# Kernel tuning notes

Measured on AMD Instinct MI355X. Metric: run time of the kernel, lower is better.

## Reference

```python
import jax, jax.numpy as jnp
import numpy as np

NEG_BIG = -9e15  # matches torch's -9000000000000000.0 masked-fill value
ALPHA = 0.2      # LeakyReLU negative slope


def setup_inputs() -> dict:
    key = jax.random.key(0)
    k1, k2, k3, k4 = jax.random.split(key, 4)
    N, F_in, F_out = 8192, 128, 64
    h = jax.random.normal(k1, (N, F_in), dtype=jnp.float32)
    adj = jax.random.randint(k2, (N, N), 0, 2).astype(jnp.float32)
    # Glorot(gain=1.414)-scale params
    W = jax.random.normal(k3, (F_in, F_out), dtype=jnp.float32) * (1.414 * np.sqrt(2.0 / (F_in + F_out)))
    a = jax.random.normal(k4, (2 * F_out, 1), dtype=jnp.float32) * (1.414 * np.sqrt(2.0 / (2 * F_out + 1)))
    return {"h": h, "adj": adj, "W": W, "a": a}


def reference(h, adj, W, a):
    F_out = W.shape[1]
    Wh = h @ W                               # [N, F_out]
    Wh1 = Wh @ a[:F_out, :]                  # [N, 1]
    Wh2 = Wh @ a[F_out:, :]                  # [N, 1]
    e = jax.nn.leaky_relu(Wh1 + Wh2.T, negative_slope=ALPHA)  # [N, N]
    attention = jnp.where(adj > 0, e, NEG_BIG)
    attention = jax.nn.softmax(attention, axis=1)
    # dropout omitted (eval mode / p applied only in training)
    h_prime = attention @ Wh                 # [N, F_out]
    return jax.nn.elu(h_prime)               # concat=True -> ELU
```

## Files before the change

### kernel.cpp

```cpp
#include <hip/hip_runtime.h>
#include <hip/hip_bf16.h>

#define N 8192
#define FIN 128
#define FOUT 64
#define ALPHA 0.2f
#define LOG2E 1.44269504f
#define JSPLIT 4
#define JSPAN (N / JSPLIT)
#define RBITS 65

typedef __attribute__((ext_vector_type(8))) short short8;
typedef __attribute__((ext_vector_type(4))) float f32x4;

static __device__ __forceinline__ unsigned fkey(float x) {
    unsigned u = __float_as_uint(x);
    return (u >> 31) ? ~u : (u | 0x80000000u);
}
static __device__ __forceinline__ float fdecode(unsigned k) {
    unsigned u = (k & 0x80000000u) ? (k & 0x7FFFFFFFu) : ~k;
    return __uint_as_float(u);
}

__global__ __launch_bounds__(256) void k_prep(const float* __restrict__ h,
                                              const float* __restrict__ W,
                                              const float* __restrict__ a,
                                              float* __restrict__ Wh,
                                              float* __restrict__ s2,
                                              float* __restrict__ t2,
                                              unsigned* __restrict__ keys) {
    __shared__ float lH[16 * FIN];
    __shared__ float lW[FIN * FOUT];
    __shared__ float red[8];
    const int tid = threadIdx.x;
    const int r0 = blockIdx.x * 16;
    {
        const float4* src = (const float4*)(h + (size_t)r0 * FIN);
        float4* dst = (float4*)lH;
        for (int i = tid; i < 16 * FIN / 4; i += 256) dst[i] = src[i];
        const float4* ws_ = (const float4*)W;
        float4* dw = (float4*)lW;
        for (int i = tid; i < FIN * FOUT / 4; i += 256) dw[i] = ws_[i];
    }
    __syncthreads();
    const int wave = tid >> 6, lane = tid & 63;
    float acc[4] = {0.f, 0.f, 0.f, 0.f};
    for (int k = 0; k < FIN; ++k) {
        float wv = lW[k * FOUT + lane];
#pragma unroll
        for (int r = 0; r < 4; ++r)
            acc[r] = fmaf(lH[(wave * 4 + r) * FIN + k], wv, acc[r]);
    }
    const float a1 = a[lane], a2 = a[FOUT + lane];
    float smx = -1e30f, tmx = -1e30f;
#pragma unroll
    for (int r = 0; r < 4; ++r) {
        int row = r0 + wave * 4 + r;
        Wh[(size_t)row * FOUT + lane] = acc[r];
        float sv = acc[r] * a1, tv = acc[r] * a2;
#pragma unroll
        for (int off = 32; off; off >>= 1) {
            sv += __shfl_xor(sv, off);
            tv += __shfl_xor(tv, off);
        }
        sv *= LOG2E; tv *= LOG2E;
        if (lane == 0) { s2[row] = sv; t2[row] = tv; }
        smx = fmaxf(smx, sv);
        tmx = fmaxf(tmx, tv);
    }
    if (lane == 0) { red[wave] = smx; red[4 + wave] = tmx; }
    __syncthreads();
    if (tid == 0) {
        float ms = fmaxf(fmaxf(red[0], red[1]), fmaxf(red[2], red[3]));
        float mt = fmaxf(fmaxf(red[4], red[5]), fmaxf(red[6], red[7]));
        atomicMax(keys + 0, fkey(ms));
        atomicMax(keys + 1, fkey(mt));
    }
}

__global__ __launch_bounds__(256) void k_pack(const float* __restrict__ Wh,
                                              __hip_bfloat16* __restrict__ WhB) {
    const int c = blockIdx.x;
    const int tn = threadIdx.x >> 6;
    const int lane = threadIdx.x & 63;
    const int quad = lane >> 4, l16 = lane & 15;
    const float* src = Wh + ((size_t)(c * 32 + quad * 8)) * FOUT + tn * 16 + l16;
    union { unsigned short u[8]; short8 v; } frag;
#pragma unroll
    for (int e = 0; e < 8; ++e) {
        __hip_bfloat16 b = __float2bfloat16(src[(size_t)e * FOUT]);
        frag.u[e] = *(unsigned short*)&b;
    }
    *(short8*)&WhB[(((size_t)c * 4 + tn) * 64 + lane) * 8] = frag.v;
}

__global__ __launch_bounds__(256) void k_bits(const float* __restrict__ adj,
                                              unsigned char* __restrict__ bits) {
    const size_t tb = (size_t)blockIdx.x * 256 + threadIdx.x;
    const float4* src = (const float4*)adj + tb * 2;
    float4 a = src[0];
    float4 b = src[1];
    unsigned m = 0;
    m |= (a.x != 0.f) ? 1u : 0u;
    m |= (a.y != 0.f) ? 2u : 0u;
    m |= (a.z != 0.f) ? 4u : 0u;
    m |= (a.w != 0.f) ? 8u : 0u;
    m |= (b.x != 0.f) ? 16u : 0u;
    m |= (b.y != 0.f) ? 32u : 0u;
    m |= (b.z != 0.f) ? 64u : 0u;
    m |= (b.w != 0.f) ? 128u : 0u;
    bits[tb] = (unsigned char)m;
}

__global__ __launch_bounds__(256) void k_attn(const unsigned* __restrict__ bits,
                                              const __hip_bfloat16* __restrict__ WhB,
                                              const float* __restrict__ s2,
                                              const float* __restrict__ t2,
                                              const unsigned* __restrict__ keys,
                                              float* __restrict__ acc_ws,
                                              float* __restrict__ l_ws) {
    __shared__ unsigned bitw[32 * RBITS];
    __shared__ float tl[JSPAN];
    __shared__ float ep[4][4][64][4];
    const int tid = threadIdx.x;
    const int wave = tid >> 6, lane = tid & 63;
    const int quad = lane >> 4, l16 = lane & 15;
    const int rg = wave >> 1, jh = wave & 1;
    const int i0 = blockIdx.x * 32;
    const int jb = blockIdx.y * JSPAN;

    for (int i = tid; i < 32 * 64; i += 256) {
        const int r = i >> 6, c = i & 63;
        bitw[r * RBITS + c] = bits[(size_t)(i0 + r) * (N / 32) + (jb >> 5) + c];
    }
    for (int i = tid; i < JSPAN / 4; i += 256)
        ((float4*)tl)[i] = ((const float4*)(t2 + jb))[i];
    __syncthreads();

    const float mraw = fdecode(keys[0]) + fdecode(keys[1]);
    const float mm = mraw > 0.f ? mraw : ALPHA * mraw;
    const int rrow = 16 * rg + l16;
    const float sm = s2[i0 + rrow];
    const short8* BF = (const short8*)WhB;
    const short8 onesv = {0x3F80, 0x3F80, 0x3F80, 0x3F80, 0x3F80, 0x3F80, 0x3F80, 0x3F80};

    f32x4 acc0 = {0,0,0,0}, acc1 = {0,0,0,0}, acc2 = {0,0,0,0}, acc3 = {0,0,0,0};
    f32x4 accL = {0,0,0,0};

    short8 Bp0[4], Bp1[4];

#define LOADB0(uu)                                                               \
    do {                                                                         \
        const int u_ = jh * 32 + ((uu) > 31 ? 31 : (uu));                        \
        const size_t kc_ = ((size_t)blockIdx.y * (JSPAN / 32) + u_) * 4;         \
        Bp0[0] = BF[(kc_ + 0) * 64 + lane];                                      \
        Bp0[1] = BF[(kc_ + 1) * 64 + lane];                                      \
        Bp0[2] = BF[(kc_ + 2) * 64 + lane];                                      \
        Bp0[3] = BF[(kc_ + 3) * 64 + lane];                                      \
    } while (0)
#define LOADB1(uu)                                                               \
    do {                                                                         \
        const int u_ = jh * 32 + ((uu) > 31 ? 31 : (uu));                        \
        const size_t kc_ = ((size_t)blockIdx.y * (JSPAN / 32) + u_) * 4;         \
        Bp1[0] = BF[(kc_ + 0) * 64 + lane];                                      \
        Bp1[1] = BF[(kc_ + 1) * 64 + lane];                                      \
        Bp1[2] = BF[(kc_ + 2) * 64 + lane];                                      \
        Bp1[3] = BF[(kc_ + 3) * 64 + lane];                                      \
    } while (0)
#define PROC(BP, uu)                                                             \
    do {                                                                         \
        const int u_ = jh * 32 + (uu);                                           \
        const unsigned bd = bitw[rrow * RBITS + u_];                             \
        const unsigned bb = (bd >> (quad * 8)) & 0xFFu;                          \
        const float* tp = &tl[u_ * 32 + quad * 8];                               \
        float4 tlo = *(const float4*)tp;                                         \
        float4 thi = *(const float4*)(tp + 4);                                   \
        union { __hip_bfloat162 h2[4]; short8 v; } af;                           \
        _Pragma("unroll")                                                        \
        for (int pp = 0; pp < 4; ++pp) {                                         \
            float t0 = (pp < 2) ? ((const float*)&tlo)[2 * pp]                   \
                                : ((const float*)&thi)[2 * pp - 4];              \
            float t1 = (pp < 2) ? ((const float*)&tlo)[2 * pp + 1]               \
                                : ((const float*)&thi)[2 * pp - 3];              \
            float x0 = sm + t0, x1 = sm + t1;                                    \
            float le0 = fmaxf(x0, ALPHA * x0), le1 = fmaxf(x1, ALPHA * x1);      \
            float e0 = exp2f(le0 - mm), e1 = exp2f(le1 - mm);                    \
            float p0 = ((bb >> (2 * pp)) & 1u) ? e0 : 0.f;                       \
            float p1 = ((bb >> (2 * pp + 1)) & 1u) ? e1 : 0.f;                   \
            af.h2[pp] = __float22bfloat162_rn(make_float2(p0, p1));              \
        }                                                                        \
        acc0 = __builtin_amdgcn_mfma_f32_16x16x32_bf16(af.v, BP[0], acc0, 0, 0, 0); \
        acc1 = __builtin_amdgcn_mfma_f32_16x16x32_bf16(af.v, BP[1], acc1, 0, 0, 0); \
        acc2 = __builtin_amdgcn_mfma_f32_16x16x32_bf16(af.v, BP[2], acc2, 0, 0, 0); \
        acc3 = __builtin_amdgcn_mfma_f32_16x16x32_bf16(af.v, BP[3], acc3, 0, 0, 0); \
        accL = __builtin_amdgcn_mfma_f32_16x16x32_bf16(af.v, onesv, accL, 0, 0, 0); \
    } while (0)

    LOADB0(0);
    LOADB1(1);
#pragma unroll 1
    for (int k = 0; k < 16; ++k) {
        PROC(Bp0, 2 * k);
        PROC(Bp1, 2 * k + 1);
        LOADB0(2 * k + 2);
        LOADB1(2 * k + 3);
    }
#undef LOADB0
#undef LOADB1
#undef PROC

    if (l16 == 0) {
#pragma unroll
        for (int r = 0; r < 4; ++r)
            atomicAdd(&l_ws[i0 + 16 * rg + quad * 4 + r], accL[r]);
    }

    *(f32x4*)&ep[wave][0][lane][0] = acc0;
    *(f32x4*)&ep[wave][1][lane][0] = acc1;
    *(f32x4*)&ep[wave][2][lane][0] = acc2;
    *(f32x4*)&ep[wave][3][lane][0] = acc3;
    __syncthreads();
    if (jh == 0) {
#pragma unroll
        for (int t = 0; t < 4; ++t) {
            f32x4 mine = *(const f32x4*)&ep[wave][t][lane][0];
            f32x4 oth  = *(const f32x4*)&ep[wave + 1][t][lane][0];
#pragma unroll
            for (int r = 0; r < 4; ++r) {
                int row = 16 * rg + quad * 4 + r;
                atomicAdd(&acc_ws[(size_t)(i0 + row) * FOUT + t * 16 + l16],
                          mine[r] + oth[r]);
            }
        }
    }
}

__global__ __launch_bounds__(256) void k_final(const float* __restrict__ acc_ws,
                                               const float* __restrict__ l_ws,
                                               float* __restrict__ out) {
    const int idx = blockIdx.x * 256 + threadIdx.x;
    const int row = idx >> 4;
    const float inv = 1.0f / l_ws[row];
    float4 a = ((const float4*)acc_ws)[idx];
    float4 o;
#pragma unroll
    for (int r = 0; r < 4; ++r) {
        float v = ((const float*)&a)[r] * inv;
        ((float*)&o)[r] = v > 0.f ? v : (exp2f(v * LOG2E) - 1.f);
    }
    ((float4*)out)[idx] = o;
}

extern "C" void kernel_launch(void* const* d_in, const int* in_sizes, int n_in,
                              void* d_out, int out_size, void* d_ws, size_t ws_size,
                              hipStream_t stream) {
    const float* h   = (const float*)d_in[0];
    const float* adj = (const float*)d_in[1];
    const float* W   = (const float*)d_in[2];
    const float* a   = (const float*)d_in[3];
    float* out = (float*)d_out;

    char* base = (char*)d_ws;
    float* Wh = (float*)base;                        base += (size_t)N * FOUT * 4;
    __hip_bfloat16* WhB = (__hip_bfloat16*)base;     base += (size_t)N * FOUT * 2;
    float* s2 = (float*)base;                        base += (size_t)N * 4;
    float* t2 = (float*)base;                        base += (size_t)N * 4;
    unsigned char* bits = (unsigned char*)base;      base += (size_t)N * N / 8;
    float* acc_ws = (float*)base;                    base += (size_t)N * FOUT * 4;
    float* l_ws = (float*)base;                      base += (size_t)N * 4;
    unsigned* keys = (unsigned*)base;

    hipMemsetAsync(acc_ws, 0, ((size_t)N * FOUT + N) * 4 + 2 * sizeof(unsigned), stream);
    k_prep<<<N / 16, 256, 0, stream>>>(h, W, a, Wh, s2, t2, keys);
    k_pack<<<N / 32, 256, 0, stream>>>(Wh, WhB);
    k_bits<<<(int)((size_t)N * N / 8 / 256), 256, 0, stream>>>(adj, bits);
    dim3 ag(N / 32, JSPLIT);
    k_attn<<<ag, 256, 0, stream>>>((const unsigned*)bits, WhB, s2, t2, keys, acc_ws, l_ws);
    k_final<<<N * FOUT / 4 / 256, 256, 0, stream>>>(acc_ws, l_ws, out);
}
```

Before: 424.5 us.

## Fuse adjacency bitmask construction into attention kernel via wave ballots

Removes the separate k_bits pass and its global bitmask buffer. Each attention block now reads its 32-row by 2048-column adj tile directly and builds the mask in shared memory with wave ballots, which needs a new interleaved bit layout and matching decode in the inner loop. Shared memory is reused for the epilogue reduction, adding an extra barrier. The adj read still dominates traffic, but the mask write and reread plus one kernel launch go away. In exchange the attention kernel's prologue gets heavier and does less overlap with compute.

```diff
diff --git a/kernel.cpp b/kernel.cpp
--- a/kernel.cpp
+++ b/kernel.cpp
@@ -8,7 +8,7 @@
 #define LOG2E 1.44269504f
 #define JSPLIT 4
 #define JSPAN (N / JSPLIT)
-#define RBITS 65
+#define RBW 68
 
 typedef __attribute__((ext_vector_type(8))) short short8;
 typedef __attribute__((ext_vector_type(4))) float f32x4;
@@ -94,34 +94,16 @@
     *(short8*)&WhB[(((size_t)c * 4 + tn) * 64 + lane) * 8] = frag.v;
 }
 
-__global__ __launch_bounds__(256) void k_bits(const float* __restrict__ adj,
-                                              unsigned char* __restrict__ bits) {
-    const size_t tb = (size_t)blockIdx.x * 256 + threadIdx.x;
-    const float4* src = (const float4*)adj + tb * 2;
-    float4 a = src[0];
-    float4 b = src[1];
-    unsigned m = 0;
-    m |= (a.x != 0.f) ? 1u : 0u;
-    m |= (a.y != 0.f) ? 2u : 0u;
-    m |= (a.z != 0.f) ? 4u : 0u;
-    m |= (a.w != 0.f) ? 8u : 0u;
-    m |= (b.x != 0.f) ? 16u : 0u;
-    m |= (b.y != 0.f) ? 32u : 0u;
-    m |= (b.z != 0.f) ? 64u : 0u;
-    m |= (b.w != 0.f) ? 128u : 0u;
-    bits[tb] = (unsigned char)m;
-}
-
-__global__ __launch_bounds__(256) void k_attn(const unsigned* __restrict__ bits,
+__global__ __launch_bounds__(256) void k_attn(const float* __restrict__ adj,
                                               const __hip_bfloat16* __restrict__ WhB,
                                               const float* __restrict__ s2,
                                               const float* __restrict__ t2,
                                               const unsigned* __restrict__ keys,
                                               float* __restrict__ acc_ws,
                                               float* __restrict__ l_ws) {
-    __shared__ unsigned bitw[32 * RBITS];
-    __shared__ float tl[JSPAN];
-    __shared__ float ep[4][4][64][4];
+    __shared__ unsigned char smem[32 * RBW * 4 + JSPAN * 4];
+    unsigned* bitw = (unsigned*)smem;
+    float* tl = (float*)(smem + 32 * RBW * 4);
     const int tid = threadIdx.x;
     const int wave = tid >> 6, lane = tid & 63;
     const int quad = lane >> 4, l16 = lane & 15;
@@ -129,12 +111,33 @@
     const int i0 = blockIdx.x * 32;
     const int jb = blockIdx.y * JSPAN;
 
-    for (int i = tid; i < 32 * 64; i += 256) {
-        const int r = i >> 6, c = i & 63;
-        bitw[r * RBITS + c] = bits[(size_t)(i0 + r) * (N / 32) + (jb >> 5) + c];
-    }
     for (int i = tid; i < JSPAN / 4; i += 256)
         ((float4*)tl)[i] = ((const float4*)(t2 + jb))[i];
+
+#pragma unroll 1
+    for (int rr = 0; rr < 8; ++rr) {
+        const int row = 8 * wave + rr;
+        const float4* src = (const float4*)(adj + (size_t)(i0 + row) * N + jb) + lane;
+        float4 v0 = src[0],   v1 = src[64],  v2 = src[128], v3 = src[192];
+        float4 v4 = src[256], v5 = src[320], v6 = src[384], v7 = src[448];
+#define BALSTEP(vv, s)                                                           \
+        do {                                                                     \
+            unsigned long long q0 = __ballot((vv).x != 0.f);                     \
+            unsigned long long q1 = __ballot((vv).y != 0.f);                     \
+            unsigned long long q2 = __ballot((vv).z != 0.f);                     \
+            unsigned long long q3 = __ballot((vv).w != 0.f);                     \
+            if (lane == 0) {                                                     \
+                unsigned* d = &bitw[row * RBW + (s) * 8];                        \
+                d[0] = (unsigned)q0; d[1] = (unsigned)q1;                        \
+                d[2] = (unsigned)q2; d[3] = (unsigned)q3;                        \
+                d[4] = (unsigned)(q0 >> 32); d[5] = (unsigned)(q1 >> 32);        \
+                d[6] = (unsigned)(q2 >> 32); d[7] = (unsigned)(q3 >> 32);        \
+            }                                                                    \
+        } while (0)
+        BALSTEP(v0, 0); BALSTEP(v1, 1); BALSTEP(v2, 2); BALSTEP(v3, 3);
+        BALSTEP(v4, 4); BALSTEP(v5, 5); BALSTEP(v6, 6); BALSTEP(v7, 7);
+#undef BALSTEP
+    }
     __syncthreads();
 
     const float mraw = fdecode(keys[0]) + fdecode(keys[1]);
@@ -170,8 +173,10 @@
 #define PROC(BP, uu)                                                             \
     do {                                                                         \
         const int u_ = jh * 32 + (uu);                                           \
-        const unsigned bd = bitw[rrow * RBITS + u_];                             \
-        const unsigned bb = (bd >> (quad * 8)) & 0xFFu;                          \
+        const int L0 = ((u_ & 7) << 3) + (quad << 1);            \
+        const int b0 = L0 & 31;                                                  \
+        const int hi = L0 >> 5;                                                  \
+        uint4 d = *(const uint4*)&bitw[rrow * RBW + (u_ >> 3) * 8 + hi * 4];     \
         const float* tp = &tl[u_ * 32 + quad * 8];                               \
         float4 tlo = *(const float4*)tp;                                         \
         float4 thi = *(const float4*)(tp + 4);                                   \
@@ -182,11 +187,14 @@
                                 : ((const float*)&thi)[2 * pp - 4];              \
             float t1 = (pp < 2) ? ((const float*)&tlo)[2 * pp + 1]               \
                                 : ((const float*)&thi)[2 * pp - 3];              \
+            const unsigned da = (pp & 1) ? d.z : d.x;                            \
+            const unsigned db = (pp & 1) ? d.w : d.y;                            \
+            const int sh = b0 + (pp >> 1);             \
             float x0 = sm + t0, x1 = sm + t1;                                    \
             float le0 = fmaxf(x0, ALPHA * x0), le1 = fmaxf(x1, ALPHA * x1);      \
             float e0 = exp2f(le0 - mm), e1 = exp2f(le1 - mm);                    \
-            float p0 = ((bb >> (2 * pp)) & 1u) ? e0 : 0.f;                       \
-            float p1 = ((bb >> (2 * pp + 1)) & 1u) ? e1 : 0.f;                   \
+            float p0 = ((da >> sh) & 1u) ? e0 : 0.f;                             \
+            float p1 = ((db >> sh) & 1u) ? e1 : 0.f;                             \
             af.h2[pp] = __float22bfloat162_rn(make_float2(p0, p1));              \
         }                                                                        \
         acc0 = __builtin_amdgcn_mfma_f32_16x16x32_bf16(af.v, BP[0], acc0, 0, 0, 0); \
@@ -215,16 +223,18 @@
             atomicAdd(&l_ws[i0 + 16 * rg + quad * 4 + r], accL[r]);
     }
 
-    *(f32x4*)&ep[wave][0][lane][0] = acc0;
-    *(f32x4*)&ep[wave][1][lane][0] = acc1;
-    *(f32x4*)&ep[wave][2][lane][0] = acc2;
-    *(f32x4*)&ep[wave][3][lane][0] = acc3;
+    __syncthreads();
+    float* ep = (float*)smem;
+    *(f32x4*)&ep[((wave * 4 + 0) * 64 + lane) * 4] = acc0;
+    *(f32x4*)&ep[((wave * 4 + 1) * 64 + lane) * 4] = acc1;
+    *(f32x4*)&ep[((wave * 4 + 2) * 64 + lane) * 4] = acc2;
+    *(f32x4*)&ep[((wave * 4 + 3) * 64 + lane) * 4] = acc3;
     __syncthreads();
     if (jh == 0) {
 #pragma unroll
         for (int t = 0; t < 4; ++t) {
-            f32x4 mine = *(const f32x4*)&ep[wave][t][lane][0];
-            f32x4 oth  = *(const f32x4*)&ep[wave + 1][t][lane][0];
+            f32x4 mine = *(const f32x4*)&ep[((wave * 4 + t) * 64 + lane) * 4];
+            f32x4 oth  = *(const f32x4*)&ep[(((wave + 1) * 4 + t) * 64 + lane) * 4];
 #pragma unroll
             for (int r = 0; r < 4; ++r) {
                 int row = 16 * rg + quad * 4 + r;
@@ -265,7 +275,6 @@
     __hip_bfloat16* WhB = (__hip_bfloat16*)base;     base += (size_t)N * FOUT * 2;
     float* s2 = (float*)base;                        base += (size_t)N * 4;
     float* t2 = (float*)base;                        base += (size_t)N * 4;
-    unsigned char* bits = (unsigned char*)base;      base += (size_t)N * N / 8;
     float* acc_ws = (float*)base;                    base += (size_t)N * FOUT * 4;
     float* l_ws = (float*)base;                      base += (size_t)N * 4;
     unsigned* keys = (unsigned*)base;
@@ -273,8 +282,7 @@
     hipMemsetAsync(acc_ws, 0, ((size_t)N * FOUT + N) * 4 + 2 * sizeof(unsigned), stream);
     k_prep<<<N / 16, 256, 0, stream>>>(h, W, a, Wh, s2, t2, keys);
     k_pack<<<N / 32, 256, 0, stream>>>(Wh, WhB);
-    k_bits<<<(int)((size_t)N * N / 8 / 256), 256, 0, stream>>>(adj, bits);
     dim3 ag(N / 32, JSPLIT);
-    k_attn<<<ag, 256, 0, stream>>>((const unsigned*)bits, WhB, s2, t2, keys, acc_ws, l_ws);
+    k_attn<<<ag, 256, 0, stream>>>(adj, WhB, s2, t2, keys, acc_ws, l_ws);
     k_final<<<N * FOUT / 4 / 256, 256, 0, stream>>>(acc_ws, l_ws, out);
 }
```

Result: no change. 427.3 us (+0.7%).
